# Performance work log

Measured on AMD Instinct MI355X. Metric: run time of the kernel, lower is better.

The kernel has to match this reference:

```python
import jax, jax.numpy as jnp
import numpy as np

NT, C, B, N, H, E = 32768, 128, 64, 512, 4, 524288  # total nodes, channels, graphs, nodes/graph, heads, edges
DH = C // H
EPS = 1e-5


def batchnorm(x, g, b):
    # BatchNorm1d over the node dimension (training-mode batch statistics)
    m = x.mean(axis=0)
    v = x.var(axis=0)
    return (x - m) * jax.lax.rsqrt(v + EPS) * g + b


def setup_inputs() -> dict:
    key = jax.random.key(0)
    ks = jax.random.split(key, 8)
    s = 1.0 / np.sqrt(C)
    return dict(
        x=jax.random.normal(ks[0], (NT, C), jnp.float32),
        edge_index=jax.random.randint(ks[1], (2, E), 0, NT, dtype=jnp.int32),
        Wc=jax.random.normal(ks[2], (C, C), jnp.float32) * s,
        bc=jnp.zeros((C,), jnp.float32),
        in_proj_w=jax.random.normal(ks[3], (3 * C, C), jnp.float32) * s,
        in_proj_b=jnp.zeros((3 * C,), jnp.float32),
        out_proj_w=jax.random.normal(ks[4], (C, C), jnp.float32) * s,
        out_proj_b=jnp.zeros((C,), jnp.float32),
        gn1=jnp.ones((C,), jnp.float32), bn1=jnp.zeros((C,), jnp.float32),
        gn2=jnp.ones((C,), jnp.float32), bn2=jnp.zeros((C,), jnp.float32),
        gn3=jnp.ones((C,), jnp.float32), bn3=jnp.zeros((C,), jnp.float32),
        Wm1=jax.random.normal(ks[5], (2 * C, C), jnp.float32) * s,
        bm1=jnp.zeros((2 * C,), jnp.float32),
        Wm2=jax.random.normal(ks[6], (C, 2 * C), jnp.float32) / np.sqrt(2 * C),
        bm2=jnp.zeros((C,), jnp.float32),
    )


def reference(x, edge_index, Wc, bc, in_proj_w, in_proj_b, out_proj_w, out_proj_b,
              gn1, bn1, gn2, bn2, gn3, bn3, Wm1, bm1, Wm2, bm2):
    # --- local branch: mean-aggregation message passing + linear + residual + BN ---
    src, dst = edge_index[0], edge_index[1]
    agg = jax.ops.segment_sum(x[src], dst, num_segments=NT)            # [NT, C]
    cnt = jax.ops.segment_sum(jnp.ones((E, 1), x.dtype), dst, num_segments=NT)
    agg = agg / jnp.maximum(cnt, 1.0)
    h_local = agg @ Wc.T + bc + x                                       # dropout p=0 -> no-op
    h_local = batchnorm(h_local, gn1, bn1)

    # --- global branch: to_dense_batch (equal-size graphs -> reshape) + MHA ---
    hd = x.reshape(B, N, C)
    qkv = hd @ in_proj_w.T + in_proj_b                                  # [B, N, 3C]
    q, k, v = jnp.split(qkv, 3, axis=-1)
    q = q.reshape(B, N, H, DH).transpose(0, 2, 1, 3)                    # [B, H, N, DH]
    k = k.reshape(B, N, H, DH).transpose(0, 2, 1, 3)
    v = v.reshape(B, N, H, DH).transpose(0, 2, 1, 3)
    scores = jnp.einsum('bhqd,bhkd->bhqk', q, k) / np.sqrt(DH)          # [B, H, N, N]
    attn = jax.nn.softmax(scores, axis=-1)
    o = jnp.einsum('bhqk,bhkd->bhqd', attn, v)                          # [B, H, N, DH]
    o = o.transpose(0, 2, 1, 3).reshape(B, N, C)
    h_attn = (o @ out_proj_w.T + out_proj_b).reshape(NT, C) + x
    h_attn = batchnorm(h_attn, gn2, bn2)

    # --- combine + MLP + final norm ---
    out = h_local + h_attn
    out = out + (jax.nn.relu(out @ Wm1.T + bm1) @ Wm2.T + bm2)
    return batchnorm(out, gn3, bn3)
```

## Files before the change

### kernel.cpp

```cpp
#include <hip/hip_runtime.h>
#include <cstddef>

#define NT    32768
#define CCH   128
#define BB    64
#define NNODE 512
#define NHEAD 4
#define DHEAD 32
#define EE    524288
#define EPS   1e-5f
#define MAXDEG 96

typedef unsigned short u16;
typedef unsigned int   u32;
typedef __attribute__((ext_vector_type(8))) short short8;
typedef __attribute__((ext_vector_type(4))) short short4v;
typedef __attribute__((ext_vector_type(4))) float f32x4;

__device__ __forceinline__ float b2f(u32 w) { return __uint_as_float(w << 16); }
__device__ __forceinline__ u16 f2b(float f) {
    u32 u = __float_as_uint(f);
    u += 0x7FFF + ((u >> 16) & 1);
    return (u16)(u >> 16);
}

__global__ __launch_bounds__(256) void convert_all(const float* __restrict__ x,
                                                   const float* __restrict__ Wc,
                                                   const float* __restrict__ Wqkv,
                                                   const float* __restrict__ Wo,
                                                   const float* __restrict__ Wm1,
                                                   const float* __restrict__ Wm2,
                                                   u16* __restrict__ xb,
                                                   u16* __restrict__ Wcb,
                                                   u16* __restrict__ Wqkvb,
                                                   u16* __restrict__ Wob,
                                                   u16* __restrict__ Wm1b,
                                                   u16* __restrict__ Wm2b) {
    int r = blockIdx.x * 256 + threadIdx.x;
    const float* src; u16* dst;
    if (r < 524288) { src = x; dst = xb; }
    else if ((r -= 524288) < 2048) { src = Wc; dst = Wcb; }
    else if ((r -= 2048) < 6144) { src = Wqkv; dst = Wqkvb; }
    else if ((r -= 6144) < 2048) { src = Wo; dst = Wob; }
    else if ((r -= 2048) < 4096) { src = Wm1; dst = Wm1b; }
    else { r -= 4096; src = Wm2; dst = Wm2b; }
    size_t base = (size_t)r * 8;
    float4 a = *(const float4*)(src + base);
    float4 b = *(const float4*)(src + base + 4);
    uint4 u;
    u.x = (u32)f2b(a.x) | ((u32)f2b(a.y) << 16);
    u.y = (u32)f2b(a.z) | ((u32)f2b(a.w) << 16);
    u.z = (u32)f2b(b.x) | ((u32)f2b(b.y) << 16);
    u.w = (u32)f2b(b.z) | ((u32)f2b(b.w) << 16);
    *(uint4*)(dst + base) = u;
}

__global__ __launch_bounds__(256) void fill_kernel(const int* __restrict__ ei,
                                                   int* __restrict__ cursor,
                                                   int* __restrict__ bucket) {
    int e = blockIdx.x * 256 + threadIdx.x;
    int src = ei[e];
    int dst = ei[EE + e];
    int pos = atomicAdd(cursor + dst, 1);
    if (pos < MAXDEG) bucket[dst * MAXDEG + pos] = src;
}

__global__ __launch_bounds__(256) void aggregate(const int* __restrict__ bucket,
                                                 const int* __restrict__ cursor,
                                                 const u16* __restrict__ xb,
                                                 u16* __restrict__ agg) {
    int ln = threadIdx.x >> 6;
    int c2 = threadIdx.x & 63;
    int n = blockIdx.x * 4 + ln;
    __shared__ int srcs[4][MAXDEG];
    int d = min(cursor[n], MAXDEG);
    if (c2 < d) srcs[ln][c2] = bucket[n * MAXDEG + c2];
    int c2b = c2 + 64;
    if (c2b < d) srcs[ln][c2b] = bucket[n * MAXDEG + c2b];
    __syncthreads();
    float s0 = 0.f, s1 = 0.f;
    for (int j = 0; j < d; ++j) {
        u32 w = *(const u32*)(xb + (size_t)srcs[ln][j] * CCH + c2 * 2);
        s0 += b2f(w & 0xffffu);
        s1 += b2f(w >> 16);
    }
    float inv = 1.0f / fmaxf((float)d, 1.0f);
    u32 out = (u32)f2b(s0 * inv) | ((u32)f2b(s1 * inv) << 16);
    *(u32*)(agg + (size_t)n * CCH + c2 * 2) = out;
}

template <bool RELU, int RESID, bool STATS>
__global__ __launch_bounds__(256) void gemm_mfma(const u16* __restrict__ A,
                                                 const u16* __restrict__ W,
                                                 const float* __restrict__ bias,
                                                 const u16* __restrict__ residb,
                                                 u16* __restrict__ outb,
                                                 float* __restrict__ sum,
                                                 float* __restrict__ sumsq,
                                                 int M, int N, int K) {
    __shared__ u16 As[128 * 32];
    __shared__ u16 Bs[128 * 32];
    __shared__ float csum[128];
    __shared__ float csq[128];
    int m0 = blockIdx.x * 128, n0 = blockIdx.y * 128;
    int tid = threadIdx.x;
    int lane = tid & 63, wave = tid >> 6;
    int wm = (wave & 1) * 64, wn = (wave >> 1) * 64;
    int l15 = lane & 15, l4 = lane >> 4;

    if (STATS) {
        if (tid < 128) { csum[tid] = 0.f; csq[tid] = 0.f; }
    }

    f32x4 zero = {0.f, 0.f, 0.f, 0.f};
    f32x4 acc[4][4];
#pragma unroll
    for (int i = 0; i < 4; ++i)
#pragma unroll
        for (int j = 0; j < 4; ++j) acc[i][j] = zero;

    int srow = tid >> 2;
    int scol = (tid & 3) * 8;

    for (int k0 = 0; k0 < K; k0 += 32) {
        uint4 a0 = *(const uint4*)(A + (size_t)(m0 + srow) * K + k0 + scol);
        uint4 a1 = *(const uint4*)(A + (size_t)(m0 + srow + 64) * K + k0 + scol);
        uint4 b0 = *(const uint4*)(W + (size_t)(n0 + srow) * K + k0 + scol);
        uint4 b1 = *(const uint4*)(W + (size_t)(n0 + srow + 64) * K + k0 + scol);
        __syncthreads();
        *(uint4*)&As[srow * 32 + scol] = a0;
        *(uint4*)&As[(srow + 64) * 32 + scol] = a1;
        *(uint4*)&Bs[srow * 32 + scol] = b0;
        *(uint4*)&Bs[(srow + 64) * 32 + scol] = b1;
        __syncthreads();
        short8 af[4], bf[4];
#pragma unroll
        for (int t = 0; t < 4; ++t) {
            af[t] = *(const short8*)&As[(wm + t * 16 + l15) * 32 + l4 * 8];
            bf[t] = *(const short8*)&Bs[(wn + t * 16 + l15) * 32 + l4 * 8];
        }
#pragma unroll
        for (int mt = 0; mt < 4; ++mt)
#pragma unroll
            for (int nt = 0; nt < 4; ++nt)
                acc[mt][nt] = __builtin_amdgcn_mfma_f32_16x16x32_bf16(af[mt], bf[nt], acc[mt][nt], 0, 0, 0);
    }

#pragma unroll
    for (int nt = 0; nt < 4; ++nt) {
        int col = n0 + wn + nt * 16 + l15;
        float bs = bias[col];
        float ps = 0.f, pq = 0.f;
#pragma unroll
        for (int mt = 0; mt < 4; ++mt) {
#pragma unroll
            for (int r = 0; r < 4; ++r) {
                int row = m0 + wm + mt * 16 + l4 * 4 + r;
                float v = acc[mt][nt][r] + bs;
                if (RESID == 2) v += b2f(residb[(size_t)row * N + col]);
                if (RELU) v = fmaxf(v, 0.0f);
                outb[(size_t)row * N + col] = f2b(v);
                if (STATS) { ps += v; pq += v * v; }
            }
        }
        if (STATS) {
            atomicAdd(&csum[wn + nt * 16 + l15], ps);
            atomicAdd(&csq[wn + nt * 16 + l15], pq);
        }
    }
    if (STATS) {
        __syncthreads();
        if (tid < 128) {
            atomicAdd(sum + n0 + tid, csum[tid]);
            atomicAdd(sumsq + n0 + tid, csq[tid]);
        }
    }
}

__global__ __launch_bounds__(256) void comb_kernel(const u16* __restrict__ X1,
                                                   const u16* __restrict__ X2,
                                                   const float* __restrict__ sum1,
                                                   const float* __restrict__ sq1,
                                                   const float* __restrict__ g1,
                                                   const float* __restrict__ bt1,
                                                   const float* __restrict__ sum2,
                                                   const float* __restrict__ sq2,
                                                   const float* __restrict__ g2,
                                                   const float* __restrict__ bt2,
                                                   u16* __restrict__ outb) {
    __shared__ float A1[128], B1[128], A2[128], B2[128];
    int t = threadIdx.x;
    {
        int c = t & 127;
        const float* sm = (t < 128) ? sum1 : sum2;
        const float* sq = (t < 128) ? sq1 : sq2;
        const float* g  = (t < 128) ? g1 : g2;
        const float* bt = (t < 128) ? bt1 : bt2;
        float m = sm[c] * (1.0f / NT);
        float v = sq[c] * (1.0f / NT) - m * m;
        float a = g[c] * rsqrtf(v + EPS);
        if (t < 128) { A1[c] = a; B1[c] = bt[c] - m * a; }
        else         { A2[c] = a; B2[c] = bt[c] - m * a; }
    }
    __syncthreads();
    int i8 = blockIdx.x * 256 + t;
    size_t i = (size_t)i8 * 8;
    int c = (int)(i & (CCH - 1));
    uint4 u1 = *(const uint4*)(X1 + i);
    uint4 u2 = *(const uint4*)(X2 + i);
    float x1[8], x2[8];
    x1[0] = b2f(u1.x & 0xffffu); x1[1] = b2f(u1.x >> 16);
    x1[2] = b2f(u1.y & 0xffffu); x1[3] = b2f(u1.y >> 16);
    x1[4] = b2f(u1.z & 0xffffu); x1[5] = b2f(u1.z >> 16);
    x1[6] = b2f(u1.w & 0xffffu); x1[7] = b2f(u1.w >> 16);
    x2[0] = b2f(u2.x & 0xffffu); x2[1] = b2f(u2.x >> 16);
    x2[2] = b2f(u2.y & 0xffffu); x2[3] = b2f(u2.y >> 16);
    x2[4] = b2f(u2.z & 0xffffu); x2[5] = b2f(u2.z >> 16);
    x2[6] = b2f(u2.w & 0xffffu); x2[7] = b2f(u2.w >> 16);
    u16 o[8];
#pragma unroll
    for (int j = 0; j < 8; ++j) {
        int cc = c + j;
        o[j] = f2b(A1[cc] * x1[j] + B1[cc] + A2[cc] * x2[j] + B2[cc]);
    }
    *(uint4*)(outb + i) = *(uint4*)o;
}

__global__ __launch_bounds__(256) void final_bn(const u16* __restrict__ X,
                                                const float* __restrict__ sum3,
                                                const float* __restrict__ sq3,
                                                const float* __restrict__ g3,
                                                const float* __restrict__ bt3,
                                                float* __restrict__ outp) {
    __shared__ float A3[128], B3[128];
    int t = threadIdx.x;
    if (t < 128) {
        float m = sum3[t] * (1.0f / NT);
        float v = sq3[t] * (1.0f / NT) - m * m;
        float a = g3[t] * rsqrtf(v + EPS);
        A3[t] = a;
        B3[t] = bt3[t] - m * a;
    }
    __syncthreads();
    int i8 = blockIdx.x * 256 + t;
    size_t i = (size_t)i8 * 8;
    int c = (int)(i & (CCH - 1));
    uint4 u = *(const uint4*)(X + i);
    float x[8];
    x[0] = b2f(u.x & 0xffffu); x[1] = b2f(u.x >> 16);
    x[2] = b2f(u.y & 0xffffu); x[3] = b2f(u.y >> 16);
    x[4] = b2f(u.z & 0xffffu); x[5] = b2f(u.z >> 16);
    x[6] = b2f(u.w & 0xffffu); x[7] = b2f(u.w >> 16);
    float4 o0, o1;
    o0.x = A3[c + 0] * x[0] + B3[c + 0];
    o0.y = A3[c + 1] * x[1] + B3[c + 1];
    o0.z = A3[c + 2] * x[2] + B3[c + 2];
    o0.w = A3[c + 3] * x[3] + B3[c + 3];
    o1.x = A3[c + 4] * x[4] + B3[c + 4];
    o1.y = A3[c + 5] * x[5] + B3[c + 5];
    o1.z = A3[c + 6] * x[6] + B3[c + 6];
    o1.w = A3[c + 7] * x[7] + B3[c + 7];
    *(float4*)(outp + i) = o0;
    *(float4*)(outp + i + 4) = o1;
}

__global__ __launch_bounds__(512) void attn_mfma(const u16* __restrict__ qkv,
                                                 u16* __restrict__ o) {
    __shared__ __align__(16) u16 Ks[512 * 40];
    __shared__ __align__(16) u16 Vt[32 * 520];
    int bh = blockIdx.x;
    int b = bh >> 2, h = bh & 3;
    int tid = threadIdx.x;
    int lane = tid & 63, wave = tid >> 6;
    int quad = lane >> 4, l15 = lane & 15;
    const float scale = 0.1767766952966369f;

    const u16* kvbase = qkv + (size_t)b * 512 * 384 + 128 + h * 32;
    for (int idx = tid; idx < 2048; idx += 512) {
        int row = idx >> 2, c = idx & 3;
        *(uint4*)&Ks[row * 40 + c * 8] = *(const uint4*)(kvbase + (size_t)row * 384 + c * 8);
    }
    for (int idx = tid; idx < 2048; idx += 512) {
        int row = idx >> 2, c = idx & 3;
        uint4 u = *(const uint4*)(kvbase + 128 + (size_t)row * 384 + c * 8);
        u16 e[8];
        *(uint4*)e = u;
#pragma unroll
        for (int i = 0; i < 8; ++i) Vt[(c * 8 + i) * 520 + row] = e[i];
    }
    __syncthreads();

    f32x4 zero = {0.f, 0.f, 0.f, 0.f};
    for (int qt = 0; qt < 4; ++qt) {
        int qbase = wave * 64 + qt * 16;
        short8 qf = *(const short8*)(qkv + (size_t)(b * 512 + qbase + l15) * 384 + h * 32 + quad * 8);
        float lq = 0.f;
        f32x4 oa[2] = {zero, zero};

        for (int kv0 = 0; kv0 < 512; kv0 += 64) {
            f32x4 s[4];
#pragma unroll
            for (int t = 0; t < 4; ++t) {
                short8 kb = *(const short8*)&Ks[(kv0 + t * 16 + l15) * 40 + quad * 8];
                s[t] = __builtin_amdgcn_mfma_f32_16x16x32_bf16(kb, qf, zero, 0, 0, 0);
            }
            short8 pa[4];
#pragma unroll
            for (int t = 0; t < 4; ++t) {
                float p0 = __expf(s[t][0] * scale);
                float p1 = __expf(s[t][1] * scale);
                float p2 = __expf(s[t][2] * scale);
                float p3 = __expf(s[t][3] * scale);
                lq += (p0 + p1) + (p2 + p3);
                short8 a8 = {(short)f2b(p0), (short)f2b(p1), (short)f2b(p2), (short)f2b(p3), 0, 0, 0, 0};
                pa[t] = a8;
            }
#pragma unroll
            for (int t = 0; t < 4; ++t) {
                int tbase = kv0 + t * 16;
#pragma unroll
                for (int n = 0; n < 2; ++n) {
                    short4v v4 = *(const short4v*)&Vt[(n * 16 + l15) * 520 + tbase + quad * 4];
                    short8 vb = {v4.x, v4.y, v4.z, v4.w, 0, 0, 0, 0};
                    oa[n] = __builtin_amdgcn_mfma_f32_16x16x32_bf16(pa[t], vb, oa[n], 0, 0, 0);
                }
            }
        }
        lq += __shfl_xor(lq, 16);
        lq += __shfl_xor(lq, 32);
        u16* op = o + (size_t)(b * 512 + qbase) * 128 + h * 32;
#pragma unroll
        for (int r = 0; r < 4; ++r) {
            float Lr = __shfl(lq, quad * 4 + r);
            float inv = 1.0f / Lr;
#pragma unroll
            for (int n = 0; n < 2; ++n)
                op[(quad * 4 + r) * 128 + n * 16 + l15] = f2b(oa[n][r] * inv);
        }
    }
}

extern "C" void kernel_launch(void* const* d_in, const int* in_sizes, int n_in,
                              void* d_out, int out_size, void* d_ws, size_t ws_size,
                              hipStream_t stream) {
    const float* x    = (const float*)d_in[0];
    const int*   ei   = (const int*)d_in[1];
    const float* Wc   = (const float*)d_in[2];
    const float* bc   = (const float*)d_in[3];
    const float* Wqkv = (const float*)d_in[4];
    const float* bqkv = (const float*)d_in[5];
    const float* Wo   = (const float*)d_in[6];
    const float* bo   = (const float*)d_in[7];
    const float* gn1  = (const float*)d_in[8];
    const float* bn1b = (const float*)d_in[9];
    const float* gn2  = (const float*)d_in[10];
    const float* bn2b = (const float*)d_in[11];
    const float* gn3  = (const float*)d_in[12];
    const float* bn3b = (const float*)d_in[13];
    const float* Wm1  = (const float*)d_in[14];
    const float* bm1  = (const float*)d_in[15];
    const float* Wm2  = (const float*)d_in[16];
    const float* bm2  = (const float*)d_in[17];
    float* outp = (float*)d_out;

    char* w = (char*)d_ws;
    const size_t MB = 1024 * 1024;
    u16* xb    = (u16*)(w);
    u16* hlocb = (u16*)(w + 8 * MB);
    u16* t2b   = (u16*)(w + 16 * MB);
    u16* out2b = (u16*)(w + 24 * MB);
    u16* qkvb  = (u16*)(w + 32 * MB);
    u16* hidb  = (u16*)(w + 56 * MB);
    u16* shb   = (u16*)(w + 72 * MB);
    int* bucket = (int*)(w + 80 * MB);
    int* cursor = (int*)(w + 92 * MB);
    float* stats = (float*)(w + 92 * MB + 128 * 1024);
    u16* Wcb   = (u16*)(w + 93 * MB);
    u16* Wqkvb = Wcb + 16384;
    u16* Wob   = Wqkvb + 49152;
    u16* Wm1b  = Wob + 16384;
    u16* Wm2b  = Wm1b + 32768;
    float* sum1 = stats;        float* sq1 = stats + 128;
    float* sum2 = stats + 256;  float* sq2 = stats + 384;
    float* sum3 = stats + 512;  float* sq3 = stats + 640;

    hipMemsetAsync(cursor, 0, 128 * 1024 + 6 * 128 * 4, stream);

    convert_all<<<2120, 256, 0, stream>>>(x, Wc, Wqkv, Wo, Wm1, Wm2,
                                          xb, Wcb, Wqkvb, Wob, Wm1b, Wm2b);

    fill_kernel<<<EE / 256, 256, 0, stream>>>(ei, cursor, bucket);
    aggregate<<<NT / 4, 256, 0, stream>>>(bucket, cursor, xb, shb);
    {
        dim3 g(NT / 128, 1);
        gemm_mfma<false, 2, true><<<g, 256, 0, stream>>>(
            shb, Wcb, bc, xb, hlocb, sum1, sq1, NT, 128, 128);
    }

    {
        dim3 g(NT / 128, 3);
        gemm_mfma<false, 0, false><<<g, 256, 0, stream>>>(
            xb, Wqkvb, bqkv, nullptr, qkvb, nullptr, nullptr, NT, 384, 128);
    }
    attn_mfma<<<BB * NHEAD, 512, 0, stream>>>(qkvb, shb);
    {
        dim3 g(NT / 128, 1);
        gemm_mfma<false, 2, true><<<g, 256, 0, stream>>>(
            shb, Wob, bo, xb, t2b, sum2, sq2, NT, 128, 128);
    }

    comb_kernel<<<NT * CCH / 8 / 256, 256, 0, stream>>>(
        hlocb, t2b, sum1, sq1, gn1, bn1b, sum2, sq2, gn2, bn2b, shb);

    {
        dim3 g(NT / 128, 2);
        gemm_mfma<true, 0, false><<<g, 256, 0, stream>>>(
            shb, Wm1b, bm1, nullptr, hidb, nullptr, nullptr, NT, 256, 128);
    }
    {
        dim3 g(NT / 128, 1);
        gemm_mfma<false, 2, true><<<g, 256, 0, stream>>>(
            hidb, Wm2b, bm2, shb, out2b, sum3, sq3, NT, 128, 256);
    }
    final_bn<<<NT * CCH / 8 / 256, 256, 0, stream>>>(out2b, sum3, sq3, gn3, bn3b, outp);
}
```

Before: 261.6 us.

## Fuse prep kernels, merge Wc+QKV GEMMs, fold BN-combine into MLP1 GEMM

Merges the bf16 conversion and the edge bucket fill into one launch. Merges the Wc GEMM and the QKV GEMM into a single grid with four y-slices. Folds the BN1/BN2 combine elementwise pass into the A-tile load of the first MLP GEMM, with the y==0 blocks also writing the combined tensor for the later residual. Widens aggregate to 4 channels per thread and 8 nodes per block. Together these remove kernel launches and one full read and write pass of the combined activations, in exchange for redundant combine arithmetic in the second column slice of MLP1 and extra branching in the merged kernels.

```diff
diff --git a/kernel.cpp b/kernel.cpp
--- a/kernel.cpp
+++ b/kernel.cpp
@@ -24,7 +24,7 @@
     return (u16)(u >> 16);
 }
 
-__global__ __launch_bounds__(256) void convert_all(const float* __restrict__ x,
+__global__ __launch_bounds__(256) void prep_kernel(const float* __restrict__ x,
                                                    const float* __restrict__ Wc,
                                                    const float* __restrict__ Wqkv,
                                                    const float* __restrict__ Wo,
@@ -35,7 +35,18 @@
                                                    u16* __restrict__ Wqkvb,
                                                    u16* __restrict__ Wob,
                                                    u16* __restrict__ Wm1b,
-                                                   u16* __restrict__ Wm2b) {
+                                                   u16* __restrict__ Wm2b,
+                                                   const int* __restrict__ ei,
+                                                   int* __restrict__ cursor,
+                                                   int* __restrict__ bucket) {
+    if (blockIdx.x >= 2120) {
+        int e = (blockIdx.x - 2120) * 256 + threadIdx.x;
+        int src = ei[e];
+        int dst = ei[EE + e];
+        int pos = atomicAdd(cursor + dst, 1);
+        if (pos < MAXDEG) bucket[dst * MAXDEG + pos] = src;
+        return;
+    }
     int r = blockIdx.x * 256 + threadIdx.x;
     const float* src; u16* dst;
     if (r < 524288) { src = x; dst = xb; }
@@ -55,38 +66,30 @@
     *(uint4*)(dst + base) = u;
 }
 
-__global__ __launch_bounds__(256) void fill_kernel(const int* __restrict__ ei,
-                                                   int* __restrict__ cursor,
-                                                   int* __restrict__ bucket) {
-    int e = blockIdx.x * 256 + threadIdx.x;
-    int src = ei[e];
-    int dst = ei[EE + e];
-    int pos = atomicAdd(cursor + dst, 1);
-    if (pos < MAXDEG) bucket[dst * MAXDEG + pos] = src;
-}
-
 __global__ __launch_bounds__(256) void aggregate(const int* __restrict__ bucket,
                                                  const int* __restrict__ cursor,
                                                  const u16* __restrict__ xb,
                                                  u16* __restrict__ agg) {
-    int ln = threadIdx.x >> 6;
-    int c2 = threadIdx.x & 63;
-    int n = blockIdx.x * 4 + ln;
-    __shared__ int srcs[4][MAXDEG];
+    int ln = threadIdx.x >> 5;
+    int c4 = threadIdx.x & 31;
+    int n = blockIdx.x * 8 + ln;
+    __shared__ int srcs[8][MAXDEG];
     int d = min(cursor[n], MAXDEG);
-    if (c2 < d) srcs[ln][c2] = bucket[n * MAXDEG + c2];
-    int c2b = c2 + 64;
-    if (c2b < d) srcs[ln][c2b] = bucket[n * MAXDEG + c2b];
+    for (int j = c4; j < d; j += 32) srcs[ln][j] = bucket[n * MAXDEG + j];
     __syncthreads();
-    float s0 = 0.f, s1 = 0.f;
+    float s0 = 0.f, s1 = 0.f, s2 = 0.f, s3 = 0.f;
     for (int j = 0; j < d; ++j) {
-        u32 w = *(const u32*)(xb + (size_t)srcs[ln][j] * CCH + c2 * 2);
-        s0 += b2f(w & 0xffffu);
-        s1 += b2f(w >> 16);
+        uint2 w = *(const uint2*)(xb + (size_t)srcs[ln][j] * CCH + c4 * 4);
+        s0 += b2f(w.x & 0xffffu);
+        s1 += b2f(w.x >> 16);
+        s2 += b2f(w.y & 0xffffu);
+        s3 += b2f(w.y >> 16);
     }
     float inv = 1.0f / fmaxf((float)d, 1.0f);
-    u32 out = (u32)f2b(s0 * inv) | ((u32)f2b(s1 * inv) << 16);
-    *(u32*)(agg + (size_t)n * CCH + c2 * 2) = out;
+    uint2 out;
+    out.x = (u32)f2b(s0 * inv) | ((u32)f2b(s1 * inv) << 16);
+    out.y = (u32)f2b(s2 * inv) | ((u32)f2b(s3 * inv) << 16);
+    *(uint2*)(agg + (size_t)n * CCH + c4 * 4) = out;
 }
 
 template <bool RELU, int RESID, bool STATS>
@@ -177,53 +180,218 @@
     }
 }
 
-__global__ __launch_bounds__(256) void comb_kernel(const u16* __restrict__ X1,
-                                                   const u16* __restrict__ X2,
-                                                   const float* __restrict__ sum1,
-                                                   const float* __restrict__ sq1,
-                                                   const float* __restrict__ g1,
-                                                   const float* __restrict__ bt1,
-                                                   const float* __restrict__ sum2,
-                                                   const float* __restrict__ sq2,
-                                                   const float* __restrict__ g2,
-                                                   const float* __restrict__ bt2,
-                                                   u16* __restrict__ outb) {
-    __shared__ float A1[128], B1[128], A2[128], B2[128];
-    int t = threadIdx.x;
+__global__ __launch_bounds__(256) void gemm_wc_qkv(const u16* __restrict__ aggb,
+                                                   const u16* __restrict__ Wcb,
+                                                   const float* __restrict__ bc,
+                                                   const u16* __restrict__ xb,
+                                                   u16* __restrict__ hlocb,
+                                                   float* __restrict__ sum1,
+                                                   float* __restrict__ sq1,
+                                                   const u16* __restrict__ Wqkvb,
+                                                   const float* __restrict__ bqkv,
+                                                   u16* __restrict__ qkvb) {
+    __shared__ u16 As[128 * 32];
+    __shared__ u16 Bs[128 * 32];
+    __shared__ float csum[128];
+    __shared__ float csq[128];
+    int y = blockIdx.y;
+    bool wc = (y == 0);
+    const u16* A = wc ? aggb : xb;
+    const u16* W = wc ? Wcb : (Wqkvb + (size_t)(y - 1) * 128 * 128);
+    const float* bias = wc ? bc : (bqkv + (y - 1) * 128);
+    int ostride = wc ? 128 : 384;
+    int ocol0 = wc ? 0 : (y - 1) * 128;
+    u16* outp = wc ? hlocb : qkvb;
+
+    int m0 = blockIdx.x * 128;
+    int tid = threadIdx.x;
+    int lane = tid & 63, wave = tid >> 6;
+    int wm = (wave & 1) * 64, wn = (wave >> 1) * 64;
+    int l15 = lane & 15, l4 = lane >> 4;
+
+    if (wc && tid < 128) { csum[tid] = 0.f; csq[tid] = 0.f; }
+
+    f32x4 zero = {0.f, 0.f, 0.f, 0.f};
+    f32x4 acc[4][4];
+#pragma unroll
+    for (int i = 0; i < 4; ++i)
+#pragma unroll
+        for (int j = 0; j < 4; ++j) acc[i][j] = zero;
+
+    int srow = tid >> 2;
+    int scol = (tid & 3) * 8;
+
+    for (int k0 = 0; k0 < 128; k0 += 32) {
+        uint4 a0 = *(const uint4*)(A + (size_t)(m0 + srow) * 128 + k0 + scol);
+        uint4 a1 = *(const uint4*)(A + (size_t)(m0 + srow + 64) * 128 + k0 + scol);
+        uint4 b0 = *(const uint4*)(W + (size_t)srow * 128 + k0 + scol);
+        uint4 b1 = *(const uint4*)(W + (size_t)(srow + 64) * 128 + k0 + scol);
+        __syncthreads();
+        *(uint4*)&As[srow * 32 + scol] = a0;
+        *(uint4*)&As[(srow + 64) * 32 + scol] = a1;
+        *(uint4*)&Bs[srow * 32 + scol] = b0;
+        *(uint4*)&Bs[(srow + 64) * 32 + scol] = b1;
+        __syncthreads();
+        short8 af[4], bf[4];
+#pragma unroll
+        for (int t = 0; t < 4; ++t) {
+            af[t] = *(const short8*)&As[(wm + t * 16 + l15) * 32 + l4 * 8];
+            bf[t] = *(const short8*)&Bs[(wn + t * 16 + l15) * 32 + l4 * 8];
+        }
+#pragma unroll
+        for (int mt = 0; mt < 4; ++mt)
+#pragma unroll
+            for (int nt = 0; nt < 4; ++nt)
+                acc[mt][nt] = __builtin_amdgcn_mfma_f32_16x16x32_bf16(af[mt], bf[nt], acc[mt][nt], 0, 0, 0);
+    }
+
+#pragma unroll
+    for (int nt = 0; nt < 4; ++nt) {
+        int lcol = wn + nt * 16 + l15;
+        float bs = bias[lcol];
+        float ps = 0.f, pq = 0.f;
+#pragma unroll
+        for (int mt = 0; mt < 4; ++mt) {
+#pragma unroll
+            for (int r = 0; r < 4; ++r) {
+                int row = m0 + wm + mt * 16 + l4 * 4 + r;
+                float v = acc[mt][nt][r] + bs;
+                if (wc) v += b2f(xb[(size_t)row * 128 + lcol]);
+                outp[(size_t)row * ostride + ocol0 + lcol] = f2b(v);
+                if (wc) { ps += v; pq += v * v; }
+            }
+        }
+        if (wc) {
+            atomicAdd(&csum[lcol], ps);
+            atomicAdd(&csq[lcol], pq);
+        }
+    }
+    if (wc) {
+        __syncthreads();
+        if (tid < 128) {
+            atomicAdd(sum1 + tid, csum[tid]);
+            atomicAdd(sq1 + tid, csq[tid]);
+        }
+    }
+}
+
+__global__ __launch_bounds__(256) void gemm_m1c(const u16* __restrict__ hlocb,
+                                                const u16* __restrict__ t2b,
+                                                const float* __restrict__ sum1,
+                                                const float* __restrict__ sq1,
+                                                const float* __restrict__ g1,
+                                                const float* __restrict__ bt1,
+                                                const float* __restrict__ sum2,
+                                                const float* __restrict__ sq2,
+                                                const float* __restrict__ g2,
+                                                const float* __restrict__ bt2,
+                                                u16* __restrict__ shb,
+                                                const u16* __restrict__ Wm1b,
+                                                const float* __restrict__ bm1,
+                                                u16* __restrict__ hidb) {
+    __shared__ u16 As[128 * 32];
+    __shared__ u16 Bs[128 * 32];
+    __shared__ float AF1[128], BF1[128], AF2[128], BF2[128];
+    int tid = threadIdx.x;
     {
-        int c = t & 127;
-        const float* sm = (t < 128) ? sum1 : sum2;
-        const float* sq = (t < 128) ? sq1 : sq2;
-        const float* g  = (t < 128) ? g1 : g2;
-        const float* bt = (t < 128) ? bt1 : bt2;
+        int c = tid & 127;
+        const float* sm = (tid < 128) ? sum1 : sum2;
+        const float* sq = (tid < 128) ? sq1 : sq2;
+        const float* g  = (tid < 128) ? g1 : g2;
+        const float* bt = (tid < 128) ? bt1 : bt2;
         float m = sm[c] * (1.0f / NT);
         float v = sq[c] * (1.0f / NT) - m * m;
         float a = g[c] * rsqrtf(v + EPS);
-        if (t < 128) { A1[c] = a; B1[c] = bt[c] - m * a; }
-        else         { A2[c] = a; B2[c] = bt[c] - m * a; }
-    }
-    __syncthreads();
-    int i8 = blockIdx.x * 256 + t;
-    size_t i = (size_t)i8 * 8;
-    int c = (int)(i & (CCH - 1));
-    uint4 u1 = *(const uint4*)(X1 + i);
-    uint4 u2 = *(const uint4*)(X2 + i);
-    float x1[8], x2[8];
-    x1[0] = b2f(u1.x & 0xffffu); x1[1] = b2f(u1.x >> 16);
-    x1[2] = b2f(u1.y & 0xffffu); x1[3] = b2f(u1.y >> 16);
-    x1[4] = b2f(u1.z & 0xffffu); x1[5] = b2f(u1.z >> 16);
-    x1[6] = b2f(u1.w & 0xffffu); x1[7] = b2f(u1.w >> 16);
-    x2[0] = b2f(u2.x & 0xffffu); x2[1] = b2f(u2.x >> 16);
-    x2[2] = b2f(u2.y & 0xffffu); x2[3] = b2f(u2.y >> 16);
-    x2[4] = b2f(u2.z & 0xffffu); x2[5] = b2f(u2.z >> 16);
-    x2[6] = b2f(u2.w & 0xffffu); x2[7] = b2f(u2.w >> 16);
-    u16 o[8];
-#pragma unroll
-    for (int j = 0; j < 8; ++j) {
-        int cc = c + j;
-        o[j] = f2b(A1[cc] * x1[j] + B1[cc] + A2[cc] * x2[j] + B2[cc]);
-    }
-    *(uint4*)(outb + i) = *(uint4*)o;
+        if (tid < 128) { AF1[c] = a; BF1[c] = bt[c] - m * a; }
+        else           { AF2[c] = a; BF2[c] = bt[c] - m * a; }
+    }
+    int m0 = blockIdx.x * 128, n0 = blockIdx.y * 128;
+    int lane = tid & 63, wave = tid >> 6;
+    int wm = (wave & 1) * 64, wn = (wave >> 1) * 64;
+    int l15 = lane & 15, l4 = lane >> 4;
+
+    f32x4 zero = {0.f, 0.f, 0.f, 0.f};
+    f32x4 acc[4][4];
+#pragma unroll
+    for (int i = 0; i < 4; ++i)
+#pragma unroll
+        for (int j = 0; j < 4; ++j) acc[i][j] = zero;
+
+    int srow = tid >> 2;
+    int scol = (tid & 3) * 8;
+    bool wr = (blockIdx.y == 0);
+
+    for (int k0 = 0; k0 < 128; k0 += 32) {
+        uint4 h0 = *(const uint4*)(hlocb + (size_t)(m0 + srow) * 128 + k0 + scol);
+        uint4 h1 = *(const uint4*)(hlocb + (size_t)(m0 + srow + 64) * 128 + k0 + scol);
+        uint4 t0 = *(const uint4*)(t2b + (size_t)(m0 + srow) * 128 + k0 + scol);
+        uint4 t1 = *(const uint4*)(t2b + (size_t)(m0 + srow + 64) * 128 + k0 + scol);
+        uint4 b0 = *(const uint4*)(Wm1b + (size_t)(n0 + srow) * 128 + k0 + scol);
+        uint4 b1 = *(const uint4*)(Wm1b + (size_t)(n0 + srow + 64) * 128 + k0 + scol);
+        __syncthreads();
+        uint4 c0, c1;
+        {
+            const u32 hw[4] = {h0.x, h0.y, h0.z, h0.w};
+            const u32 tw[4] = {t0.x, t0.y, t0.z, t0.w};
+            u32 ow[4];
+#pragma unroll
+            for (int p = 0; p < 4; ++p) {
+                int cc = k0 + scol + p * 2;
+                float v0 = AF1[cc] * b2f(hw[p] & 0xffffu) + BF1[cc] + AF2[cc] * b2f(tw[p] & 0xffffu) + BF2[cc];
+                float v1 = AF1[cc + 1] * b2f(hw[p] >> 16) + BF1[cc + 1] + AF2[cc + 1] * b2f(tw[p] >> 16) + BF2[cc + 1];
+                ow[p] = (u32)f2b(v0) | ((u32)f2b(v1) << 16);
+            }
+            c0.x = ow[0]; c0.y = ow[1]; c0.z = ow[2]; c0.w = ow[3];
+        }
+        {
+            const u32 hw[4] = {h1.x, h1.y, h1.z, h1.w};
+            const u32 tw[4] = {t1.x, t1.y, t1.z, t1.w};
+            u32 ow[4];
+#pragma unroll
+            for (int p = 0; p < 4; ++p) {
+                int cc = k0 + scol + p * 2;
+                float v0 = AF1[cc] * b2f(hw[p] & 0xffffu) + BF1[cc] + AF2[cc] * b2f(tw[p] & 0xffffu) + BF2[cc];
+                float v1 = AF1[cc + 1] * b2f(hw[p] >> 16) + BF1[cc + 1] + AF2[cc + 1] * b2f(tw[p] >> 16) + BF2[cc + 1];
+                ow[p] = (u32)f2b(v0) | ((u32)f2b(v1) << 16);
+            }
+            c1.x = ow[0]; c1.y = ow[1]; c1.z = ow[2]; c1.w = ow[3];
+        }
+        *(uint4*)&As[srow * 32 + scol] = c0;
+        *(uint4*)&As[(srow + 64) * 32 + scol] = c1;
+        *(uint4*)&Bs[srow * 32 + scol] = b0;
+        *(uint4*)&Bs[(srow + 64) * 32 + scol] = b1;
+        if (wr) {
+            *(uint4*)(shb + (size_t)(m0 + srow) * 128 + k0 + scol) = c0;
+            *(uint4*)(shb + (size_t)(m0 + srow + 64) * 128 + k0 + scol) = c1;
+        }
+        __syncthreads();
+        short8 af[4], bf[4];
+#pragma unroll
+        for (int t = 0; t < 4; ++t) {
+            af[t] = *(const short8*)&As[(wm + t * 16 + l15) * 32 + l4 * 8];
+            bf[t] = *(const short8*)&Bs[(wn + t * 16 + l15) * 32 + l4 * 8];
+        }
+#pragma unroll
+        for (int mt = 0; mt < 4; ++mt)
+#pragma unroll
+            for (int nt = 0; nt < 4; ++nt)
+                acc[mt][nt] = __builtin_amdgcn_mfma_f32_16x16x32_bf16(af[mt], bf[nt], acc[mt][nt], 0, 0, 0);
+    }
+
+#pragma unroll
+    for (int nt = 0; nt < 4; ++nt) {
+        int col = n0 + wn + nt * 16 + l15;
+        float bs = bm1[col];
+#pragma unroll
+        for (int mt = 0; mt < 4; ++mt) {
+#pragma unroll
+            for (int r = 0; r < 4; ++r) {
+                int row = m0 + wm + mt * 16 + l4 * 4 + r;
+                float v = fmaxf(acc[mt][nt][r] + bs, 0.0f);
+                hidb[(size_t)row * 256 + col] = f2b(v);
+            }
+        }
+    }
 }
 
 __global__ __launch_bounds__(256) void final_bn(const u16* __restrict__ X,
@@ -386,41 +554,37 @@
 
     hipMemsetAsync(cursor, 0, 128 * 1024 + 6 * 128 * 4, stream);
 
-    convert_all<<<2120, 256, 0, stream>>>(x, Wc, Wqkv, Wo, Wm1, Wm2,
-                                          xb, Wcb, Wqkvb, Wob, Wm1b, Wm2b);
-
-    fill_kernel<<<EE / 256, 256, 0, stream>>>(ei, cursor, bucket);
-    aggregate<<<NT / 4, 256, 0, stream>>>(bucket, cursor, xb, shb);
+    prep_kernel<<<2120 + 2048, 256, 0, stream>>>(x, Wc, Wqkv, Wo, Wm1, Wm2,
+                                                 xb, Wcb, Wqkvb, Wob, Wm1b, Wm2b,
+                                                 ei, cursor, bucket);
+
+    aggregate<<<NT / 8, 256, 0, stream>>>(bucket, cursor, xb, shb);
+
     {
-        dim3 g(NT / 128, 1);
-        gemm_mfma<false, 2, true><<<g, 256, 0, stream>>>(
-            shb, Wcb, bc, xb, hlocb, sum1, sq1, NT, 128, 128);
-    }
-
-    {
-        dim3 g(NT / 128, 3);
-        gemm_mfma<false, 0, false><<<g, 256, 0, stream>>>(
-            xb, Wqkvb, bqkv, nullptr, qkvb, nullptr, nullptr, NT, 384, 128);
-    }
+        dim3 g(NT / 128, 4);
+        gemm_wc_qkv<<<g, 256, 0, stream>>>(shb, Wcb, bc, xb, hlocb, sum1, sq1,
+                                           Wqkvb, bqkv, qkvb);
+    }
+
     attn_mfma<<<BB * NHEAD, 512, 0, stream>>>(qkvb, shb);
+
     {
         dim3 g(NT / 128, 1);
         gemm_mfma<false, 2, true><<<g, 256, 0, stream>>>(
             shb, Wob, bo, xb, t2b, sum2, sq2, NT, 128, 128);
     }
 
-    comb_kernel<<<NT * CCH / 8 / 256, 256, 0, stream>>>(
-        hlocb, t2b, sum1, sq1, gn1, bn1b, sum2, sq2, gn2, bn2b, shb);
-
     {
         dim3 g(NT / 128, 2);
-        gemm_mfma<true, 0, false><<<g, 256, 0, stream>>>(
-            shb, Wm1b, bm1, nullptr, hidb, nullptr, nullptr, NT, 256, 128);
-    }
+        gemm_m1c<<<g, 256, 0, stream>>>(hlocb, t2b, sum1, sq1, gn1, bn1b,
+                                        sum2, sq2, gn2, bn2b, shb, Wm1b, bm1, hidb);
+    }
+
     {
         dim3 g(NT / 128, 1);
         gemm_mfma<false, 2, true><<<g, 256, 0, stream>>>(
             hidb, Wm2b, bm2, shb, out2b, sum3, sq3, NT, 128, 256);
     }
+
     final_bn<<<NT * CCH / 8 / 256, 256, 0, stream>>>(out2b, sum3, sq3, gn3, bn3b, outp);
 }
```

After: 254.6 us. -2.7%, faster.
